# Kernel optimization log

Hardware: AMD Instinct MI355X
Metric: run time of the kernel (lower is better)

Reference implementation:

```python
import jax, jax.numpy as jnp
import numpy as np

RADIUS = 0.5
K = 32
EPS = 1e-5


def ball_query(pc, new_pc, radius, k):
    """pc [B,3,N], new_pc [B,3,S] -> idx [B,S,k] int32, num [B,S] int32.
    First k in-radius points per query; empty slots filled with the first
    found index (standard ball-query semantics of QueryDepthPoint)."""
    d2 = jnp.sum((new_pc[:, :, :, None] - pc[:, :, None, :]) ** 2, axis=1)  # [B,S,N]
    B, S, N = d2.shape
    mask = d2 < radius * radius
    rank = jnp.cumsum(mask.astype(jnp.int32), axis=-1) - 1          # rank among valid
    slot = jnp.where(mask & (rank < k), rank, k)                     # k = dummy slot
    jidx = jnp.broadcast_to(jnp.arange(N, dtype=jnp.int32), (B, S, N))
    bidx = jnp.arange(B)[:, None, None]
    sidx = jnp.arange(S)[None, :, None]
    idx = jnp.zeros((B, S, k + 1), jnp.int32).at[bidx, sidx, slot].set(jidx)
    idx = idx[..., :k]
    num = jnp.sum(mask, axis=-1).astype(jnp.int32)                   # [B,S]
    nvalid = jnp.minimum(num, k)
    idx = jnp.where(jnp.arange(k) < nvalid[..., None], idx, idx[..., :1])
    return idx, num


def conv_bn_relu(x, w, b, g, be):
    """1x1 Conv2d + BatchNorm2d (batch stats, training mode) + ReLU.
    x [B,Cin,S,K], w [Cout,Cin]."""
    y = jnp.einsum('bcsk,oc->bosk', x, w) + b[None, :, None, None]
    mean = jnp.mean(y, axis=(0, 2, 3), keepdims=True)
    var = jnp.var(y, axis=(0, 2, 3), keepdims=True)
    y = (y - mean) * jax.lax.rsqrt(var + EPS) * g[None, :, None, None] + be[None, :, None, None]
    return jax.nn.relu(y)


def setup_inputs() -> dict:
    key = jax.random.key(0)
    ks = jax.random.split(key, 8)
    B, N, S, C = 4, 8192, 2048, 16
    mlp = [32, 32, 64]
    cin = C + 3  # use_xyz concat
    pc = jax.random.normal(ks[0], (B, 3, N), jnp.float32)
    feat = jax.random.normal(ks[1], (B, C, N), jnp.float32)
    new_pc = jax.random.normal(ks[2], (B, 3, S), jnp.float32)
    def kaiming(k, co, ci):
        return jax.random.normal(k, (co, ci), jnp.float32) * np.sqrt(2.0 / ci)
    w1 = kaiming(ks[3], mlp[0], cin)
    w2 = kaiming(ks[4], mlp[1], mlp[0])
    w3 = kaiming(ks[5], mlp[2], mlp[1])
    return {
        'pc': pc, 'feat': feat, 'new_pc': new_pc,
        'w1': w1, 'b1': jnp.zeros((mlp[0],)), 'g1': jnp.ones((mlp[0],)), 'be1': jnp.zeros((mlp[0],)),
        'w2': w2, 'b2': jnp.zeros((mlp[1],)), 'g2': jnp.ones((mlp[1],)), 'be2': jnp.zeros((mlp[1],)),
        'w3': w3, 'b3': jnp.zeros((mlp[2],)), 'g3': jnp.ones((mlp[2],)), 'be3': jnp.zeros((mlp[2],)),
    }


def reference(pc, feat, new_pc, w1, b1, g1, be1, w2, b2, g2, be2, w3, b3, g3, be3):
    B = pc.shape[0]
    S = new_pc.shape[2]
    idx, num = ball_query(pc, new_pc, RADIUS, K)          # [B,S,K], [B,S]
    bidx = jnp.arange(B)[:, None, None]
    # gather neighbors: fancy index -> [B,S,K,3] / [B,S,K,Cf], then to channel-first
    grouped_pc = pc[bidx, :, idx].transpose(0, 3, 1, 2)   # [B,3,S,K]
    grouped_pc = grouped_pc - new_pc[:, :, :, None]       # center on query
    grouped_feat = feat[bidx, :, idx].transpose(0, 3, 1, 2)  # [B,Cf,S,K]
    x = jnp.concatenate([grouped_pc, grouped_feat], axis=1)  # [B,Cf+3,S,K]
    x = conv_bn_relu(x, w1, b1, g1, be1)
    x = conv_bn_relu(x, w2, b2, g2, be2)
    x = conv_bn_relu(x, w3, b3, g3, be3)
    valid = (num > 0).astype(x.dtype)[:, None, :, None]   # [B,1,S,1]
    return x * valid
```

## Files before the change

### kernel.cpp

```cpp
#include <hip/hip_runtime.h>

#define BQ_RADIUS2 0.25f
#define KK 32
#define NB 4
#define NP 8192
#define NS 2048
#define C1 32
#define C2 32
#define C3 64
#define EPSBN 1e-5f
#define RTOT 65536
#define MTOT (NB*NS*KK)
#define NSLOT 32

#define OFF_G     0
#define OFF_IDX   655360
#define OFF_VALID 917504
#define OFF_P1    925696
#define OFF_P2    927744
#define OFF_P3    929792
#define OFF_PAR1  933888
#define OFF_PAR2  933952
#define OFF_PAR3  934016

__global__ __launch_bounds__(256) void k_pack(const float* __restrict__ pc,
                                              const float* __restrict__ feat,
                                              float* __restrict__ g,
                                              float* __restrict__ partials) {
  const int t = blockIdx.x * 256 + threadIdx.x;
  if (t < 8192) partials[t] = 0.f;
  const int b = t >> 13;
  const int j = t & (NP - 1);
  const float* pcb = pc + b * 3 * NP;
  float* gp = g + (size_t)t * 20;
  gp[0] = pcb[j];
  gp[1] = pcb[NP + j];
  gp[2] = pcb[2 * NP + j];
  const float* fb = feat + b * 16 * NP;
#pragma unroll
  for (int c = 0; c < 16; c++) gp[3 + c] = fb[c * NP + j];
  gp[19] = 0.f;
}

__global__ __launch_bounds__(256) void k_ballquery(const float* __restrict__ pc,
                                                   const float* __restrict__ newpc,
                                                   int* __restrict__ idx,
                                                   int* __restrict__ valid) {
  __shared__ int buf[4][KK];
  const int tid = threadIdx.x;
  const int w = tid >> 6, lane = tid & 63;
  const int gq = blockIdx.x * 4 + w;
  const int b = gq >> 11, s = gq & (NS - 1);
  const float* np0 = newpc + b * 3 * NS;
  const float qx = np0[s], qy = np0[NS + s], qz = np0[2 * NS + s];
  const float* px = pc + b * 3 * NP;
  const float* py = px + NP;
  const float* pz = px + 2 * NP;
  if (lane == 0) buf[w][0] = 0;
  int cnt = 0;
  for (int j0 = 0; j0 < NP; j0 += 256) {
    const int jb = j0 + lane * 4;
    const float4 vx = *(const float4*)(px + jb);
    const float4 vy = *(const float4*)(py + jb);
    const float4 vz = *(const float4*)(pz + jb);
    int mm = 0;
    {
      float dx = __fsub_rn(qx, vx.x), dy = __fsub_rn(qy, vy.x), dz = __fsub_rn(qz, vz.x);
      if (__fadd_rn(__fadd_rn(__fmul_rn(dx, dx), __fmul_rn(dy, dy)), __fmul_rn(dz, dz)) < BQ_RADIUS2) mm |= 1;
    }
    {
      float dx = __fsub_rn(qx, vx.y), dy = __fsub_rn(qy, vy.y), dz = __fsub_rn(qz, vz.y);
      if (__fadd_rn(__fadd_rn(__fmul_rn(dx, dx), __fmul_rn(dy, dy)), __fmul_rn(dz, dz)) < BQ_RADIUS2) mm |= 2;
    }
    {
      float dx = __fsub_rn(qx, vx.z), dy = __fsub_rn(qy, vy.z), dz = __fsub_rn(qz, vz.z);
      if (__fadd_rn(__fadd_rn(__fmul_rn(dx, dx), __fmul_rn(dy, dy)), __fmul_rn(dz, dz)) < BQ_RADIUS2) mm |= 4;
    }
    {
      float dx = __fsub_rn(qx, vx.w), dy = __fsub_rn(qy, vy.w), dz = __fsub_rn(qz, vz.w);
      if (__fadd_rn(__fadd_rn(__fmul_rn(dx, dx), __fmul_rn(dy, dy)), __fmul_rn(dz, dz)) < BQ_RADIUS2) mm |= 8;
    }
    const int c4 = __popc(mm);
    int pre = c4;
#pragma unroll
    for (int off = 1; off < 64; off <<= 1) {
      int v = __shfl_up(pre, off);
      if (lane >= off) pre += v;
    }
    const int total = __shfl(pre, 63);
    if (mm) {
      int base = cnt + pre - c4;
#pragma unroll
      for (int i = 0; i < 4; i++) {
        if ((mm >> i) & 1) {
          if (base < KK) buf[w][base] = jb + i;
          base++;
        }
      }
    }
    cnt += total;
    if (cnt >= KK) break;
  }
  __syncthreads();
  if (lane < KK) {
    const int f = cnt < KK ? cnt : KK;
    const int i0 = buf[w][0];
    idx[gq * KK + lane] = (lane < f) ? buf[w][lane] : i0;
  }
  if (lane == 0) valid[gq] = (cnt > 0);
}

__global__ __launch_bounds__(256, 1) void k_conv1(const float* __restrict__ g,
                                                  const int* __restrict__ idx,
                                                  const float* __restrict__ newpc,
                                                  const float* __restrict__ w1,
                                                  const float* __restrict__ b1,
                                                  float* __restrict__ y,
                                                  float* __restrict__ partial) {
  __shared__ float wl[C1 * 20];
  __shared__ float bl[C1];
  __shared__ float red[16][2 * C1 + 1];
  const int tid = threadIdx.x;
  for (int i = tid; i < C1 * 20; i += 256) {
    const int o = i / 20, c = i - o * 20;
    wl[i] = (c < 19) ? w1[o * 19 + c] : 0.f;
  }
  if (tid < C1) bl[tid] = b1[tid];
  __syncthreads();
  const int pos = blockIdx.x * 256 + tid;
  const int p4 = pos << 2;
  const int b = p4 >> 16;
  const int r = p4 & (RTOT - 1);
  const int s = r >> 5;
  const int4 jj = *(const int4*)(idx + p4);
  const float* np0 = newpc + b * 3 * NS;
  const float nx = np0[s], ny = np0[NS + s], nz = np0[2 * NS + s];
  float4 xr[20];
#define LOADPT(COMP, J) { \
    const float4* gp = (const float4*)(g + (size_t)(b * NP + (J)) * 20); \
    const float4 a0 = gp[0], a1 = gp[1], a2 = gp[2], a3 = gp[3], a4 = gp[4]; \
    xr[0].COMP = a0.x - nx; xr[1].COMP = a0.y - ny; xr[2].COMP = a0.z - nz; xr[3].COMP = a0.w; \
    xr[4].COMP = a1.x; xr[5].COMP = a1.y; xr[6].COMP = a1.z; xr[7].COMP = a1.w; \
    xr[8].COMP = a2.x; xr[9].COMP = a2.y; xr[10].COMP = a2.z; xr[11].COMP = a2.w; \
    xr[12].COMP = a3.x; xr[13].COMP = a3.y; xr[14].COMP = a3.z; xr[15].COMP = a3.w; \
    xr[16].COMP = a4.x; xr[17].COMP = a4.y; xr[18].COMP = a4.z; xr[19].COMP = a4.w; }
  LOADPT(x, jj.x) LOADPT(y, jj.y) LOADPT(z, jj.z) LOADPT(w, jj.w)
#undef LOADPT
  float* yb = y + ((size_t)b * C3) * RTOT + r;
  const int grp = tid >> 4;
  const bool lead = (tid & 15) == 0;
#pragma unroll 4
  for (int o = 0; o < C1; o++) {
    const float bo = bl[o];
    float4 acc = make_float4(bo, bo, bo, bo);
    const float4* wr = (const float4*)&wl[o * 20];
#pragma unroll
    for (int ct = 0; ct < 5; ct++) {
      const float4 wv = wr[ct];
      const float4 x0 = xr[4 * ct + 0], x1 = xr[4 * ct + 1], x2 = xr[4 * ct + 2], x3 = xr[4 * ct + 3];
      acc.x = fmaf(wv.x, x0.x, acc.x); acc.y = fmaf(wv.x, x0.y, acc.y);
      acc.z = fmaf(wv.x, x0.z, acc.z); acc.w = fmaf(wv.x, x0.w, acc.w);
      acc.x = fmaf(wv.y, x1.x, acc.x); acc.y = fmaf(wv.y, x1.y, acc.y);
      acc.z = fmaf(wv.y, x1.z, acc.z); acc.w = fmaf(wv.y, x1.w, acc.w);
      acc.x = fmaf(wv.z, x2.x, acc.x); acc.y = fmaf(wv.z, x2.y, acc.y);
      acc.z = fmaf(wv.z, x2.z, acc.z); acc.w = fmaf(wv.z, x2.w, acc.w);
      acc.x = fmaf(wv.w, x3.x, acc.x); acc.y = fmaf(wv.w, x3.y, acc.y);
      acc.z = fmaf(wv.w, x3.z, acc.z); acc.w = fmaf(wv.w, x3.w, acc.w);
    }
    *(float4*)(yb + (size_t)o * RTOT) = acc;
    float a = (acc.x + acc.y) + (acc.z + acc.w);
    float q = (acc.x * acc.x + acc.y * acc.y) + (acc.z * acc.z + acc.w * acc.w);
    a += __shfl_xor(a, 1); q += __shfl_xor(q, 1);
    a += __shfl_xor(a, 2); q += __shfl_xor(q, 2);
    a += __shfl_xor(a, 4); q += __shfl_xor(q, 4);
    a += __shfl_xor(a, 8); q += __shfl_xor(q, 8);
    if (lead) { red[grp][o] = a; red[grp][C1 + o] = q; }
  }
  __syncthreads();
  if (tid < 2 * C1) {
    float v = 0.f;
#pragma unroll
    for (int gq = 0; gq < 16; gq++) v += red[gq][tid];
    atomicAdd(&partial[(blockIdx.x & (NSLOT - 1)) * 2 * C1 + tid], v);
  }
}

__global__ __launch_bounds__(256, 1) void k_conv2(const float* __restrict__ w2,
                                                  const float* __restrict__ b2,
                                                  const float* __restrict__ par,
                                                  float* y,
                                                  float* __restrict__ partial) {
  __shared__ float wl[C2 * C1];
  __shared__ float bl[C2];
  __shared__ float pl[2 * C1];
  __shared__ float red[16][2 * C2 + 1];
  const int tid = threadIdx.x;
  for (int i = tid; i < C2 * C1; i += 256) wl[i] = w2[i];
  if (tid < C2) bl[tid] = b2[tid];
  if (tid < 2 * C1) pl[tid] = par[tid];
  __syncthreads();
  const int pos = blockIdx.x * 256 + tid;
  const int p4 = pos << 2;
  const int b = p4 >> 16;
  const int r = p4 & (RTOT - 1);
  float* yb = y + ((size_t)b * C3) * RTOT + r;
  float4 xr[C1];
#pragma unroll
  for (int c = 0; c < C1; c++) {
    float4 v = *(const float4*)(yb + (size_t)c * RTOT);
    const float sc = pl[c], sh = pl[C1 + c];
    v.x = fmaxf(fmaf(v.x, sc, sh), 0.f);
    v.y = fmaxf(fmaf(v.y, sc, sh), 0.f);
    v.z = fmaxf(fmaf(v.z, sc, sh), 0.f);
    v.w = fmaxf(fmaf(v.w, sc, sh), 0.f);
    xr[c] = v;
  }
  const int grp = tid >> 4;
  const bool lead = (tid & 15) == 0;
#pragma unroll 4
  for (int o = 0; o < C2; o++) {
    const float bo = bl[o];
    float4 acc = make_float4(bo, bo, bo, bo);
    const float4* wr = (const float4*)&wl[o * C1];
#pragma unroll
    for (int ct = 0; ct < C1 / 4; ct++) {
      const float4 wv = wr[ct];
      const float4 x0 = xr[4 * ct + 0], x1 = xr[4 * ct + 1], x2 = xr[4 * ct + 2], x3 = xr[4 * ct + 3];
      acc.x = fmaf(wv.x, x0.x, acc.x); acc.y = fmaf(wv.x, x0.y, acc.y);
      acc.z = fmaf(wv.x, x0.z, acc.z); acc.w = fmaf(wv.x, x0.w, acc.w);
      acc.x = fmaf(wv.y, x1.x, acc.x); acc.y = fmaf(wv.y, x1.y, acc.y);
      acc.z = fmaf(wv.y, x1.z, acc.z); acc.w = fmaf(wv.y, x1.w, acc.w);
      acc.x = fmaf(wv.z, x2.x, acc.x); acc.y = fmaf(wv.z, x2.y, acc.y);
      acc.z = fmaf(wv.z, x2.z, acc.z); acc.w = fmaf(wv.z, x2.w, acc.w);
      acc.x = fmaf(wv.w, x3.x, acc.x); acc.y = fmaf(wv.w, x3.y, acc.y);
      acc.z = fmaf(wv.w, x3.z, acc.z); acc.w = fmaf(wv.w, x3.w, acc.w);
    }
    *(float4*)(yb + (size_t)o * RTOT) = acc;
    float a = (acc.x + acc.y) + (acc.z + acc.w);
    float q = (acc.x * acc.x + acc.y * acc.y) + (acc.z * acc.z + acc.w * acc.w);
    a += __shfl_xor(a, 1); q += __shfl_xor(q, 1);
    a += __shfl_xor(a, 2); q += __shfl_xor(q, 2);
    a += __shfl_xor(a, 4); q += __shfl_xor(q, 4);
    a += __shfl_xor(a, 8); q += __shfl_xor(q, 8);
    if (lead) { red[grp][o] = a; red[grp][C2 + o] = q; }
  }
  __syncthreads();
  if (tid < 2 * C2) {
    float v = 0.f;
#pragma unroll
    for (int gq = 0; gq < 16; gq++) v += red[gq][tid];
    atomicAdd(&partial[(blockIdx.x & (NSLOT - 1)) * 2 * C2 + tid], v);
  }
}

__global__ __launch_bounds__(256, 1) void k_conv3(const float* __restrict__ w3,
                                                  const float* __restrict__ b3,
                                                  const float* __restrict__ par,
                                                  float* y,
                                                  float* __restrict__ partial) {
  __shared__ float wl[C3 * C2];
  __shared__ float bl[C3];
  __shared__ float pl[2 * C2];
  __shared__ float red[16][2 * C3 + 1];
  const int tid = threadIdx.x;
  for (int i = tid; i < C3 * C2; i += 256) wl[i] = w3[i];
  if (tid < C3) bl[tid] = b3[tid];
  if (tid < 2 * C2) pl[tid] = par[tid];
  __syncthreads();
  const int pos = blockIdx.x * 256 + tid;
  const int p4 = pos << 2;
  const int b = p4 >> 16;
  const int r = p4 & (RTOT - 1);
  float* yb = y + ((size_t)b * C3) * RTOT + r;
  float4 xr[C2];
#pragma unroll
  for (int c = 0; c < C2; c++) {
    float4 v = *(const float4*)(yb + (size_t)c * RTOT);
    const float sc = pl[c], sh = pl[C2 + c];
    v.x = fmaxf(fmaf(v.x, sc, sh), 0.f);
    v.y = fmaxf(fmaf(v.y, sc, sh), 0.f);
    v.z = fmaxf(fmaf(v.z, sc, sh), 0.f);
    v.w = fmaxf(fmaf(v.w, sc, sh), 0.f);
    xr[c] = v;
  }
  const int grp = tid >> 4;
  const bool lead = (tid & 15) == 0;
#pragma unroll 4
  for (int o = 0; o < C3; o++) {
    const float bo = bl[o];
    float4 acc = make_float4(bo, bo, bo, bo);
    const float4* wr = (const float4*)&wl[o * C2];
#pragma unroll
    for (int ct = 0; ct < C2 / 4; ct++) {
      const float4 wv = wr[ct];
      const float4 x0 = xr[4 * ct + 0], x1 = xr[4 * ct + 1], x2 = xr[4 * ct + 2], x3 = xr[4 * ct + 3];
      acc.x = fmaf(wv.x, x0.x, acc.x); acc.y = fmaf(wv.x, x0.y, acc.y);
      acc.z = fmaf(wv.x, x0.z, acc.z); acc.w = fmaf(wv.x, x0.w, acc.w);
      acc.x = fmaf(wv.y, x1.x, acc.x); acc.y = fmaf(wv.y, x1.y, acc.y);
      acc.z = fmaf(wv.y, x1.z, acc.z); acc.w = fmaf(wv.y, x1.w, acc.w);
      acc.x = fmaf(wv.z, x2.x, acc.x); acc.y = fmaf(wv.z, x2.y, acc.y);
      acc.z = fmaf(wv.z, x2.z, acc.z); acc.w = fmaf(wv.z, x2.w, acc.w);
      acc.x = fmaf(wv.w, x3.x, acc.x); acc.y = fmaf(wv.w, x3.y, acc.y);
      acc.z = fmaf(wv.w, x3.z, acc.z); acc.w = fmaf(wv.w, x3.w, acc.w);
    }
    *(float4*)(yb + (size_t)o * RTOT) = acc;
    float a = (acc.x + acc.y) + (acc.z + acc.w);
    float q = (acc.x * acc.x + acc.y * acc.y) + (acc.z * acc.z + acc.w * acc.w);
    a += __shfl_xor(a, 1); q += __shfl_xor(q, 1);
    a += __shfl_xor(a, 2); q += __shfl_xor(q, 2);
    a += __shfl_xor(a, 4); q += __shfl_xor(q, 4);
    a += __shfl_xor(a, 8); q += __shfl_xor(q, 8);
    if (lead) { red[grp][o] = a; red[grp][C3 + o] = q; }
  }
  __syncthreads();
  if (tid < 2 * C3) {
    float v = 0.f;
#pragma unroll
    for (int gq = 0; gq < 16; gq++) v += red[gq][tid];
    atomicAdd(&partial[(blockIdx.x & (NSLOT - 1)) * 2 * C3 + tid], v);
  }
}

__global__ void k_params(const float* __restrict__ partial,
                         const float* __restrict__ gamma,
                         const float* __restrict__ beta,
                         float* __restrict__ params, int C) {
  __shared__ float tot[2 * C3];
  const int t = threadIdx.x;
  float v = 0.f;
#pragma unroll 1
  for (int sl = 0; sl < NSLOT; ++sl) v += partial[sl * 2 * C + t];
  tot[t] = v;
  __syncthreads();
  if (t < C) {
    const float inv = 1.0f / (float)MTOT;
    const float mean = tot[t] * inv;
    const float ex2 = tot[C + t] * inv;
    const float var = ex2 - mean * mean;
    const float sc = gamma[t] * rsqrtf(var + EPSBN);
    params[t] = sc;
    params[C + t] = beta[t] - mean * sc;
  }
}

__global__ __launch_bounds__(256) void k_final(float* __restrict__ out,
                                               const float* __restrict__ par,
                                               const int* __restrict__ valid) {
  const int t = blockIdx.x * 256 + threadIdx.x;
  const size_t e = (size_t)t * 4;
  const int b = t >> 20;
  const int o = (t >> 14) & 63;
  const int s = (t & 16383) >> 3;
  const float sc = par[o], sh = par[C3 + o];
  const float m = valid[(b << 11) + s] ? 1.f : 0.f;
  float4 v = *(float4*)(out + e);
  v.x = fmaxf(fmaf(v.x, sc, sh), 0.f) * m;
  v.y = fmaxf(fmaf(v.y, sc, sh), 0.f) * m;
  v.z = fmaxf(fmaf(v.z, sc, sh), 0.f) * m;
  v.w = fmaxf(fmaf(v.w, sc, sh), 0.f) * m;
  *(float4*)(out + e) = v;
}

extern "C" void kernel_launch(void* const* d_in, const int* in_sizes, int n_in,
                              void* d_out, int out_size, void* d_ws, size_t ws_size,
                              hipStream_t stream) {
  const float* pc    = (const float*)d_in[0];
  const float* feat  = (const float*)d_in[1];
  const float* newpc = (const float*)d_in[2];
  const float* w1 = (const float*)d_in[3];
  const float* b1 = (const float*)d_in[4];
  const float* g1 = (const float*)d_in[5];
  const float* be1 = (const float*)d_in[6];
  const float* w2 = (const float*)d_in[7];
  const float* b2 = (const float*)d_in[8];
  const float* g2 = (const float*)d_in[9];
  const float* be2 = (const float*)d_in[10];
  const float* w3 = (const float*)d_in[11];
  const float* b3 = (const float*)d_in[12];
  const float* g3 = (const float*)d_in[13];
  const float* be3 = (const float*)d_in[14];

  float* ws = (float*)d_ws;
  float* gbuf  = ws + OFF_G;
  int*   idx   = (int*)(ws + OFF_IDX);
  int*   valid = (int*)(ws + OFF_VALID);
  float* p1 = ws + OFF_P1;
  float* p2 = ws + OFF_P2;
  float* p3 = ws + OFF_P3;
  float* par1 = ws + OFF_PAR1;
  float* par2 = ws + OFF_PAR2;
  float* par3 = ws + OFF_PAR3;
  float* out = (float*)d_out;

  k_pack<<<dim3(128), dim3(256), 0, stream>>>(pc, feat, gbuf, p1);
  k_ballquery<<<dim3(2048), dim3(256), 0, stream>>>(pc, newpc, idx, valid);
  k_conv1<<<dim3(256), dim3(256), 0, stream>>>(gbuf, idx, newpc, w1, b1, out, p1);
  k_params<<<dim3(1), dim3(2 * C1), 0, stream>>>(p1, g1, be1, par1, C1);
  k_conv2<<<dim3(256), dim3(256), 0, stream>>>(w2, b2, par1, out, p2);
  k_params<<<dim3(1), dim3(2 * C2), 0, stream>>>(p2, g2, be2, par2, C2);
  k_conv3<<<dim3(256), dim3(256), 0, stream>>>(w3, b3, par2, out, p3);
  k_params<<<dim3(1), dim3(2 * C3), 0, stream>>>(p3, g3, be3, par3, C3);
  k_final<<<dim3(16384), dim3(256), 0, stream>>>(out, par3, valid);
}
```

Before: 247.6 us.

## Split conv output channels across waves and fold BN params into next conv

Each 256-thread block of the three conv kernels now covers 64 position-quads instead of 256. Its four waves each compute a quarter of the output channels for the same positions, which quadruples the grid to 1024 blocks and allows two blocks per CU. The aim is more occupancy and better latency hiding than one block per CU gave. The separate k_params launches after conv1 and conv2 are removed: every block recomputes the BN scale and shift from the partial sums, which saves two tiny serial launches. The cost is redundant gathers and input reads across the four waves, plus an extra barrier before the in-place overwrite of the activations.

```diff
diff --git a/kernel.cpp b/kernel.cpp
--- a/kernel.cpp
+++ b/kernel.cpp
@@ -110,7 +110,7 @@
   if (lane == 0) valid[gq] = (cnt > 0);
 }
 
-__global__ __launch_bounds__(256, 1) void k_conv1(const float* __restrict__ g,
+__global__ __launch_bounds__(256, 2) void k_conv1(const float* __restrict__ g,
                                                   const int* __restrict__ idx,
                                                   const float* __restrict__ newpc,
                                                   const float* __restrict__ w1,
@@ -119,7 +119,7 @@
                                                   float* __restrict__ partial) {
   __shared__ float wl[C1 * 20];
   __shared__ float bl[C1];
-  __shared__ float red[16][2 * C1 + 1];
+  __shared__ float red[2 * C1];
   const int tid = threadIdx.x;
   for (int i = tid; i < C1 * 20; i += 256) {
     const int o = i / 20, c = i - o * 20;
@@ -127,8 +127,9 @@
   }
   if (tid < C1) bl[tid] = b1[tid];
   __syncthreads();
-  const int pos = blockIdx.x * 256 + tid;
-  const int p4 = pos << 2;
+  const int w = tid >> 6, lane = tid & 63;
+  const int cg = blockIdx.x * 64 + lane;
+  const int p4 = cg << 2;
   const int b = p4 >> 16;
   const int r = p4 & (RTOT - 1);
   const int s = r >> 5;
@@ -147,10 +148,10 @@
   LOADPT(x, jj.x) LOADPT(y, jj.y) LOADPT(z, jj.z) LOADPT(w, jj.w)
 #undef LOADPT
   float* yb = y + ((size_t)b * C3) * RTOT + r;
-  const int grp = tid >> 4;
-  const bool lead = (tid & 15) == 0;
+  const int o0 = w * (C1 / 4);
 #pragma unroll 4
-  for (int o = 0; o < C1; o++) {
+  for (int oi = 0; oi < C1 / 4; oi++) {
+    const int o = o0 + oi;
     const float bo = bl[o];
     float4 acc = make_float4(bo, bo, bo, bo);
     const float4* wr = (const float4*)&wl[o * 20];
@@ -170,37 +171,53 @@
     *(float4*)(yb + (size_t)o * RTOT) = acc;
     float a = (acc.x + acc.y) + (acc.z + acc.w);
     float q = (acc.x * acc.x + acc.y * acc.y) + (acc.z * acc.z + acc.w * acc.w);
-    a += __shfl_xor(a, 1); q += __shfl_xor(q, 1);
-    a += __shfl_xor(a, 2); q += __shfl_xor(q, 2);
-    a += __shfl_xor(a, 4); q += __shfl_xor(q, 4);
-    a += __shfl_xor(a, 8); q += __shfl_xor(q, 8);
-    if (lead) { red[grp][o] = a; red[grp][C1 + o] = q; }
-  }
-  __syncthreads();
-  if (tid < 2 * C1) {
-    float v = 0.f;
-#pragma unroll
-    for (int gq = 0; gq < 16; gq++) v += red[gq][tid];
-    atomicAdd(&partial[(blockIdx.x & (NSLOT - 1)) * 2 * C1 + tid], v);
-  }
-}
-
-__global__ __launch_bounds__(256, 1) void k_conv2(const float* __restrict__ w2,
+    a += __shfl_xor(a, 1);  q += __shfl_xor(q, 1);
+    a += __shfl_xor(a, 2);  q += __shfl_xor(q, 2);
+    a += __shfl_xor(a, 4);  q += __shfl_xor(q, 4);
+    a += __shfl_xor(a, 8);  q += __shfl_xor(q, 8);
+    a += __shfl_xor(a, 16); q += __shfl_xor(q, 16);
+    a += __shfl_xor(a, 32); q += __shfl_xor(q, 32);
+    if (lane == 0) { red[o] = a; red[C1 + o] = q; }
+  }
+  __syncthreads();
+  if (tid < 2 * C1)
+    atomicAdd(&partial[(blockIdx.x & (NSLOT - 1)) * 2 * C1 + tid], red[tid]);
+}
+
+__global__ __launch_bounds__(256, 2) void k_conv2(const float* __restrict__ w2,
                                                   const float* __restrict__ b2,
-                                                  const float* __restrict__ par,
+                                                  const float* __restrict__ p1,
+                                                  const float* __restrict__ g1,
+                                                  const float* __restrict__ be1,
                                                   float* y,
                                                   float* __restrict__ partial) {
   __shared__ float wl[C2 * C1];
   __shared__ float bl[C2];
   __shared__ float pl[2 * C1];
-  __shared__ float red[16][2 * C2 + 1];
+  __shared__ float tot[2 * C1];
+  __shared__ float red[2 * C2];
   const int tid = threadIdx.x;
   for (int i = tid; i < C2 * C1; i += 256) wl[i] = w2[i];
   if (tid < C2) bl[tid] = b2[tid];
-  if (tid < 2 * C1) pl[tid] = par[tid];
-  __syncthreads();
-  const int pos = blockIdx.x * 256 + tid;
-  const int p4 = pos << 2;
+  if (tid < 2 * C1) {
+    float v = 0.f;
+#pragma unroll 1
+    for (int sl = 0; sl < NSLOT; ++sl) v += p1[sl * 2 * C1 + tid];
+    tot[tid] = v;
+  }
+  __syncthreads();
+  if (tid < C1) {
+    const float inv = 1.0f / (float)MTOT;
+    const float mean = tot[tid] * inv;
+    const float var = tot[C1 + tid] * inv - mean * mean;
+    const float sc = g1[tid] * rsqrtf(var + EPSBN);
+    pl[tid] = sc;
+    pl[C1 + tid] = be1[tid] - mean * sc;
+  }
+  __syncthreads();
+  const int w = tid >> 6, lane = tid & 63;
+  const int cg = blockIdx.x * 64 + lane;
+  const int p4 = cg << 2;
   const int b = p4 >> 16;
   const int r = p4 & (RTOT - 1);
   float* yb = y + ((size_t)b * C3) * RTOT + r;
@@ -215,10 +232,11 @@
     v.w = fmaxf(fmaf(v.w, sc, sh), 0.f);
     xr[c] = v;
   }
-  const int grp = tid >> 4;
-  const bool lead = (tid & 15) == 0;
+  __syncthreads();
+  const int o0 = w * (C2 / 4);
 #pragma unroll 4
-  for (int o = 0; o < C2; o++) {
+  for (int oi = 0; oi < C2 / 4; oi++) {
+    const int o = o0 + oi;
     const float bo = bl[o];
     float4 acc = make_float4(bo, bo, bo, bo);
     const float4* wr = (const float4*)&wl[o * C1];
@@ -238,37 +256,53 @@
     *(float4*)(yb + (size_t)o * RTOT) = acc;
     float a = (acc.x + acc.y) + (acc.z + acc.w);
     float q = (acc.x * acc.x + acc.y * acc.y) + (acc.z * acc.z + acc.w * acc.w);
-    a += __shfl_xor(a, 1); q += __shfl_xor(q, 1);
-    a += __shfl_xor(a, 2); q += __shfl_xor(q, 2);
-    a += __shfl_xor(a, 4); q += __shfl_xor(q, 4);
-    a += __shfl_xor(a, 8); q += __shfl_xor(q, 8);
-    if (lead) { red[grp][o] = a; red[grp][C2 + o] = q; }
-  }
-  __syncthreads();
-  if (tid < 2 * C2) {
-    float v = 0.f;
-#pragma unroll
-    for (int gq = 0; gq < 16; gq++) v += red[gq][tid];
-    atomicAdd(&partial[(blockIdx.x & (NSLOT - 1)) * 2 * C2 + tid], v);
-  }
-}
-
-__global__ __launch_bounds__(256, 1) void k_conv3(const float* __restrict__ w3,
+    a += __shfl_xor(a, 1);  q += __shfl_xor(q, 1);
+    a += __shfl_xor(a, 2);  q += __shfl_xor(q, 2);
+    a += __shfl_xor(a, 4);  q += __shfl_xor(q, 4);
+    a += __shfl_xor(a, 8);  q += __shfl_xor(q, 8);
+    a += __shfl_xor(a, 16); q += __shfl_xor(q, 16);
+    a += __shfl_xor(a, 32); q += __shfl_xor(q, 32);
+    if (lane == 0) { red[o] = a; red[C2 + o] = q; }
+  }
+  __syncthreads();
+  if (tid < 2 * C2)
+    atomicAdd(&partial[(blockIdx.x & (NSLOT - 1)) * 2 * C2 + tid], red[tid]);
+}
+
+__global__ __launch_bounds__(256, 2) void k_conv3(const float* __restrict__ w3,
                                                   const float* __restrict__ b3,
-                                                  const float* __restrict__ par,
+                                                  const float* __restrict__ p2,
+                                                  const float* __restrict__ g2,
+                                                  const float* __restrict__ be2,
                                                   float* y,
                                                   float* __restrict__ partial) {
   __shared__ float wl[C3 * C2];
   __shared__ float bl[C3];
   __shared__ float pl[2 * C2];
-  __shared__ float red[16][2 * C3 + 1];
+  __shared__ float tot[2 * C2];
+  __shared__ float red[2 * C3];
   const int tid = threadIdx.x;
   for (int i = tid; i < C3 * C2; i += 256) wl[i] = w3[i];
   if (tid < C3) bl[tid] = b3[tid];
-  if (tid < 2 * C2) pl[tid] = par[tid];
-  __syncthreads();
-  const int pos = blockIdx.x * 256 + tid;
-  const int p4 = pos << 2;
+  if (tid < 2 * C2) {
+    float v = 0.f;
+#pragma unroll 1
+    for (int sl = 0; sl < NSLOT; ++sl) v += p2[sl * 2 * C2 + tid];
+    tot[tid] = v;
+  }
+  __syncthreads();
+  if (tid < C2) {
+    const float inv = 1.0f / (float)MTOT;
+    const float mean = tot[tid] * inv;
+    const float var = tot[C2 + tid] * inv - mean * mean;
+    const float sc = g2[tid] * rsqrtf(var + EPSBN);
+    pl[tid] = sc;
+    pl[C2 + tid] = be2[tid] - mean * sc;
+  }
+  __syncthreads();
+  const int w = tid >> 6, lane = tid & 63;
+  const int cg = blockIdx.x * 64 + lane;
+  const int p4 = cg << 2;
   const int b = p4 >> 16;
   const int r = p4 & (RTOT - 1);
   float* yb = y + ((size_t)b * C3) * RTOT + r;
@@ -283,10 +317,11 @@
     v.w = fmaxf(fmaf(v.w, sc, sh), 0.f);
     xr[c] = v;
   }
-  const int grp = tid >> 4;
-  const bool lead = (tid & 15) == 0;
+  __syncthreads();
+  const int o0 = w * (C3 / 4);
 #pragma unroll 4
-  for (int o = 0; o < C3; o++) {
+  for (int oi = 0; oi < C3 / 4; oi++) {
+    const int o = o0 + oi;
     const float bo = bl[o];
     float4 acc = make_float4(bo, bo, bo, bo);
     const float4* wr = (const float4*)&wl[o * C2];
@@ -306,19 +341,17 @@
     *(float4*)(yb + (size_t)o * RTOT) = acc;
     float a = (acc.x + acc.y) + (acc.z + acc.w);
     float q = (acc.x * acc.x + acc.y * acc.y) + (acc.z * acc.z + acc.w * acc.w);
-    a += __shfl_xor(a, 1); q += __shfl_xor(q, 1);
-    a += __shfl_xor(a, 2); q += __shfl_xor(q, 2);
-    a += __shfl_xor(a, 4); q += __shfl_xor(q, 4);
-    a += __shfl_xor(a, 8); q += __shfl_xor(q, 8);
-    if (lead) { red[grp][o] = a; red[grp][C3 + o] = q; }
-  }
-  __syncthreads();
-  if (tid < 2 * C3) {
-    float v = 0.f;
-#pragma unroll
-    for (int gq = 0; gq < 16; gq++) v += red[gq][tid];
-    atomicAdd(&partial[(blockIdx.x & (NSLOT - 1)) * 2 * C3 + tid], v);
-  }
+    a += __shfl_xor(a, 1);  q += __shfl_xor(q, 1);
+    a += __shfl_xor(a, 2);  q += __shfl_xor(q, 2);
+    a += __shfl_xor(a, 4);  q += __shfl_xor(q, 4);
+    a += __shfl_xor(a, 8);  q += __shfl_xor(q, 8);
+    a += __shfl_xor(a, 16); q += __shfl_xor(q, 16);
+    a += __shfl_xor(a, 32); q += __shfl_xor(q, 32);
+    if (lane == 0) { red[o] = a; red[C3 + o] = q; }
+  }
+  __syncthreads();
+  if (tid < 2 * C3)
+    atomicAdd(&partial[(blockIdx.x & (NSLOT - 1)) * 2 * C3 + tid], red[tid]);
 }
 
 __global__ void k_params(const float* __restrict__ partial,
@@ -387,18 +420,14 @@
   float* p1 = ws + OFF_P1;
   float* p2 = ws + OFF_P2;
   float* p3 = ws + OFF_P3;
-  float* par1 = ws + OFF_PAR1;
-  float* par2 = ws + OFF_PAR2;
   float* par3 = ws + OFF_PAR3;
   float* out = (float*)d_out;
 
   k_pack<<<dim3(128), dim3(256), 0, stream>>>(pc, feat, gbuf, p1);
   k_ballquery<<<dim3(2048), dim3(256), 0, stream>>>(pc, newpc, idx, valid);
-  k_conv1<<<dim3(256), dim3(256), 0, stream>>>(gbuf, idx, newpc, w1, b1, out, p1);
-  k_params<<<dim3(1), dim3(2 * C1), 0, stream>>>(p1, g1, be1, par1, C1);
-  k_conv2<<<dim3(256), dim3(256), 0, stream>>>(w2, b2, par1, out, p2);
-  k_params<<<dim3(1), dim3(2 * C2), 0, stream>>>(p2, g2, be2, par2, C2);
-  k_conv3<<<dim3(256), dim3(256), 0, stream>>>(w3, b3, par2, out, p3);
+  k_conv1<<<dim3(1024), dim3(256), 0, stream>>>(gbuf, idx, newpc, w1, b1, out, p1);
+  k_conv2<<<dim3(1024), dim3(256), 0, stream>>>(w2, b2, p1, g1, be1, out, p2);
+  k_conv3<<<dim3(1024), dim3(256), 0, stream>>>(w3, b3, p2, g2, be2, out, p3);
   k_params<<<dim3(1), dim3(2 * C3), 0, stream>>>(p3, g3, be3, par3, C3);
   k_final<<<dim3(16384), dim3(256), 0, stream>>>(out, par3, valid);
 }
```

Result: slower. 258.5 us (+4.4%).

## Fuse conv/BN stages into one persistent kernel with grid-wide barriers

Applied to the files above, without the earlier changes.

Replaces the three conv kernels, three BN-param kernels and the final activation kernel with a single persistent kernel of 256 blocks × 1024 threads. Each thread keeps one point's activations in registers across all three layers, and a software grid barrier on an atomic counter separates the batch-statistics reductions. This removes the intermediate global writes and reads of y and the extra launches. In exchange it relies on all 256 blocks being co-resident, carries about 128 live floats per thread, reads weights from global instead of shared memory, and writes output with one scalar store per element.

```diff
diff --git a/kernel.cpp b/kernel.cpp
--- a/kernel.cpp
+++ b/kernel.cpp
@@ -12,6 +12,7 @@
 #define RTOT 65536
 #define MTOT (NB*NS*KK)
 #define NSLOT 32
+#define NBLK 256
 
 #define OFF_G     0
 #define OFF_IDX   655360
@@ -19,16 +20,14 @@
 #define OFF_P1    925696
 #define OFF_P2    927744
 #define OFF_P3    929792
-#define OFF_PAR1  933888
-#define OFF_PAR2  933952
-#define OFF_PAR3  934016
+#define OFF_BAR   933888
 
 __global__ __launch_bounds__(256) void k_pack(const float* __restrict__ pc,
                                               const float* __restrict__ feat,
                                               float* __restrict__ g,
                                               float* __restrict__ partials) {
   const int t = blockIdx.x * 256 + threadIdx.x;
-  if (t < 8192) partials[t] = 0.f;
+  if (t < 8194) partials[t] = 0.f;
   const int b = t >> 13;
   const int j = t & (NP - 1);
   const float* pcb = pc + b * 3 * NP;
@@ -110,255 +109,158 @@
   if (lane == 0) valid[gq] = (cnt > 0);
 }
 
-__global__ __launch_bounds__(256, 1) void k_conv1(const float* __restrict__ g,
-                                                  const int* __restrict__ idx,
-                                                  const float* __restrict__ newpc,
-                                                  const float* __restrict__ w1,
-                                                  const float* __restrict__ b1,
-                                                  float* __restrict__ y,
-                                                  float* __restrict__ partial) {
-  __shared__ float wl[C1 * 20];
-  __shared__ float bl[C1];
-  __shared__ float red[16][2 * C1 + 1];
+__device__ __forceinline__ void gbar(int* bar, int tid) {
+  __syncthreads();
+  if (tid == 0) {
+    __threadfence();
+    int* gen = bar + 1;
+    const int g = __hip_atomic_load(gen, __ATOMIC_ACQUIRE, __HIP_MEMORY_SCOPE_AGENT);
+    const int a = __hip_atomic_fetch_add(bar, 1, __ATOMIC_ACQ_REL, __HIP_MEMORY_SCOPE_AGENT);
+    if (a == NBLK - 1) {
+      __hip_atomic_store(bar, 0, __ATOMIC_RELAXED, __HIP_MEMORY_SCOPE_AGENT);
+      __hip_atomic_fetch_add(gen, 1, __ATOMIC_RELEASE, __HIP_MEMORY_SCOPE_AGENT);
+    } else {
+      while (__hip_atomic_load(gen, __ATOMIC_ACQUIRE, __HIP_MEMORY_SCOPE_AGENT) == g)
+        __builtin_amdgcn_s_sleep(8);
+    }
+  }
+  __syncthreads();
+}
+
+template <int C>
+__device__ __forceinline__ void block_stats(const float* y, float (*red)[16],
+                                            float* __restrict__ partial,
+                                            int tid, int bid) {
+  const int w = tid >> 6, lane = tid & 63;
+#pragma unroll
+  for (int c = 0; c < C; c++) {
+    float a = y[c];
+    float q = a * a;
+    a += __shfl_xor(a, 1);  q += __shfl_xor(q, 1);
+    a += __shfl_xor(a, 2);  q += __shfl_xor(q, 2);
+    a += __shfl_xor(a, 4);  q += __shfl_xor(q, 4);
+    a += __shfl_xor(a, 8);  q += __shfl_xor(q, 8);
+    a += __shfl_xor(a, 16); q += __shfl_xor(q, 16);
+    a += __shfl_xor(a, 32); q += __shfl_xor(q, 32);
+    if (lane == 0) { red[c][w] = a; red[C + c][w] = q; }
+  }
+  __syncthreads();
+  if (tid < 2 * C) {
+    float v = 0.f;
+#pragma unroll
+    for (int ww = 0; ww < 16; ww++) v += red[tid][ww];
+    atomicAdd(&partial[(bid & (NSLOT - 1)) * 2 * C + tid], v);
+  }
+}
+
+template <int C>
+__device__ __forceinline__ void bn_params(const float* __restrict__ partial,
+                                          const float* __restrict__ gam,
+                                          const float* __restrict__ bet,
+                                          float* pl, float* tot, int tid) {
+  if (tid < 2 * C) {
+    float v = 0.f;
+#pragma unroll 1
+    for (int sl = 0; sl < NSLOT; ++sl) v += partial[sl * 2 * C + tid];
+    tot[tid] = v;
+  }
+  __syncthreads();
+  if (tid < C) {
+    const float inv = 1.0f / (float)MTOT;
+    const float mean = tot[tid] * inv;
+    const float var = tot[C + tid] * inv - mean * mean;
+    const float sc = gam[tid] * rsqrtf(var + EPSBN);
+    pl[tid] = sc;
+    pl[C + tid] = bet[tid] - mean * sc;
+  }
+  __syncthreads();
+}
+
+__global__ __launch_bounds__(1024, 4) void k_mega(
+    const float* __restrict__ g, const int* __restrict__ idx,
+    const float* __restrict__ newpc,
+    const float* __restrict__ w1, const float* __restrict__ b1,
+    const float* __restrict__ g1, const float* __restrict__ be1,
+    const float* __restrict__ w2, const float* __restrict__ b2,
+    const float* __restrict__ g2, const float* __restrict__ be2,
+    const float* __restrict__ w3, const float* __restrict__ b3,
+    const float* __restrict__ g3, const float* __restrict__ be3,
+    const int* __restrict__ valid,
+    float* __restrict__ p1, float* __restrict__ p2, float* __restrict__ p3,
+    float* __restrict__ out, int* bar) {
+  __shared__ float red[2 * C3][16];
+  __shared__ float tot[2 * C3];
+  __shared__ float pl[2 * C3];
   const int tid = threadIdx.x;
-  for (int i = tid; i < C1 * 20; i += 256) {
-    const int o = i / 20, c = i - o * 20;
-    wl[i] = (c < 19) ? w1[o * 19 + c] : 0.f;
-  }
-  if (tid < C1) bl[tid] = b1[tid];
-  __syncthreads();
-  const int pos = blockIdx.x * 256 + tid;
-  const int p4 = pos << 2;
-  const int b = p4 >> 16;
-  const int r = p4 & (RTOT - 1);
+  const int bid = blockIdx.x;
+
+  const int m = bid * 1024 + tid;
+  const int b = m >> 16;
+  const int r = m & (RTOT - 1);
   const int s = r >> 5;
-  const int4 jj = *(const int4*)(idx + p4);
+  const int j = idx[m];
   const float* np0 = newpc + b * 3 * NS;
-  const float nx = np0[s], ny = np0[NS + s], nz = np0[2 * NS + s];
-  float4 xr[20];
-#define LOADPT(COMP, J) { \
-    const float4* gp = (const float4*)(g + (size_t)(b * NP + (J)) * 20); \
-    const float4 a0 = gp[0], a1 = gp[1], a2 = gp[2], a3 = gp[3], a4 = gp[4]; \
-    xr[0].COMP = a0.x - nx; xr[1].COMP = a0.y - ny; xr[2].COMP = a0.z - nz; xr[3].COMP = a0.w; \
-    xr[4].COMP = a1.x; xr[5].COMP = a1.y; xr[6].COMP = a1.z; xr[7].COMP = a1.w; \
-    xr[8].COMP = a2.x; xr[9].COMP = a2.y; xr[10].COMP = a2.z; xr[11].COMP = a2.w; \
-    xr[12].COMP = a3.x; xr[13].COMP = a3.y; xr[14].COMP = a3.z; xr[15].COMP = a3.w; \
-    xr[16].COMP = a4.x; xr[17].COMP = a4.y; xr[18].COMP = a4.z; xr[19].COMP = a4.w; }
-  LOADPT(x, jj.x) LOADPT(y, jj.y) LOADPT(z, jj.z) LOADPT(w, jj.w)
-#undef LOADPT
-  float* yb = y + ((size_t)b * C3) * RTOT + r;
-  const int grp = tid >> 4;
-  const bool lead = (tid & 15) == 0;
-#pragma unroll 4
+
+  float x[19];
+  {
+    const float4* gp = (const float4*)(g + (size_t)(b * NP + j) * 20);
+    const float4 a0 = gp[0], a1 = gp[1], a2 = gp[2], a3 = gp[3], a4 = gp[4];
+    x[0] = a0.x - np0[s]; x[1] = a0.y - np0[NS + s]; x[2] = a0.z - np0[2 * NS + s];
+    x[3] = a0.w;
+    x[4] = a1.x; x[5] = a1.y; x[6] = a1.z; x[7] = a1.w;
+    x[8] = a2.x; x[9] = a2.y; x[10] = a2.z; x[11] = a2.w;
+    x[12] = a3.x; x[13] = a3.y; x[14] = a3.z; x[15] = a3.w;
+    x[16] = a4.x; x[17] = a4.y; x[18] = a4.z;
+  }
+
+  float y1[C1];
+#pragma unroll
   for (int o = 0; o < C1; o++) {
-    const float bo = bl[o];
-    float4 acc = make_float4(bo, bo, bo, bo);
-    const float4* wr = (const float4*)&wl[o * 20];
-#pragma unroll
-    for (int ct = 0; ct < 5; ct++) {
-      const float4 wv = wr[ct];
-      const float4 x0 = xr[4 * ct + 0], x1 = xr[4 * ct + 1], x2 = xr[4 * ct + 2], x3 = xr[4 * ct + 3];
-      acc.x = fmaf(wv.x, x0.x, acc.x); acc.y = fmaf(wv.x, x0.y, acc.y);
-      acc.z = fmaf(wv.x, x0.z, acc.z); acc.w = fmaf(wv.x, x0.w, acc.w);
-      acc.x = fmaf(wv.y, x1.x, acc.x); acc.y = fmaf(wv.y, x1.y, acc.y);
-      acc.z = fmaf(wv.y, x1.z, acc.z); acc.w = fmaf(wv.y, x1.w, acc.w);
-      acc.x = fmaf(wv.z, x2.x, acc.x); acc.y = fmaf(wv.z, x2.y, acc.y);
-      acc.z = fmaf(wv.z, x2.z, acc.z); acc.w = fmaf(wv.z, x2.w, acc.w);
-      acc.x = fmaf(wv.w, x3.x, acc.x); acc.y = fmaf(wv.w, x3.y, acc.y);
-      acc.z = fmaf(wv.w, x3.z, acc.z); acc.w = fmaf(wv.w, x3.w, acc.w);
-    }
-    *(float4*)(yb + (size_t)o * RTOT) = acc;
-    float a = (acc.x + acc.y) + (acc.z + acc.w);
-    float q = (acc.x * acc.x + acc.y * acc.y) + (acc.z * acc.z + acc.w * acc.w);
-    a += __shfl_xor(a, 1); q += __shfl_xor(q, 1);
-    a += __shfl_xor(a, 2); q += __shfl_xor(q, 2);
-    a += __shfl_xor(a, 4); q += __shfl_xor(q, 4);
-    a += __shfl_xor(a, 8); q += __shfl_xor(q, 8);
-    if (lead) { red[grp][o] = a; red[grp][C1 + o] = q; }
-  }
-  __syncthreads();
-  if (tid < 2 * C1) {
-    float v = 0.f;
-#pragma unroll
-    for (int gq = 0; gq < 16; gq++) v += red[gq][tid];
-    atomicAdd(&partial[(blockIdx.x & (NSLOT - 1)) * 2 * C1 + tid], v);
-  }
-}
-
-__global__ __launch_bounds__(256, 1) void k_conv2(const float* __restrict__ w2,
-                                                  const float* __restrict__ b2,
-                                                  const float* __restrict__ par,
-                                                  float* y,
-                                                  float* __restrict__ partial) {
-  __shared__ float wl[C2 * C1];
-  __shared__ float bl[C2];
-  __shared__ float pl[2 * C1];
-  __shared__ float red[16][2 * C2 + 1];
-  const int tid = threadIdx.x;
-  for (int i = tid; i < C2 * C1; i += 256) wl[i] = w2[i];
-  if (tid < C2) bl[tid] = b2[tid];
-  if (tid < 2 * C1) pl[tid] = par[tid];
-  __syncthreads();
-  const int pos = blockIdx.x * 256 + tid;
-  const int p4 = pos << 2;
-  const int b = p4 >> 16;
-  const int r = p4 & (RTOT - 1);
-  float* yb = y + ((size_t)b * C3) * RTOT + r;
-  float4 xr[C1];
-#pragma unroll
-  for (int c = 0; c < C1; c++) {
-    float4 v = *(const float4*)(yb + (size_t)c * RTOT);
-    const float sc = pl[c], sh = pl[C1 + c];
-    v.x = fmaxf(fmaf(v.x, sc, sh), 0.f);
-    v.y = fmaxf(fmaf(v.y, sc, sh), 0.f);
-    v.z = fmaxf(fmaf(v.z, sc, sh), 0.f);
-    v.w = fmaxf(fmaf(v.w, sc, sh), 0.f);
-    xr[c] = v;
-  }
-  const int grp = tid >> 4;
-  const bool lead = (tid & 15) == 0;
-#pragma unroll 4
+    float acc = b1[o];
+    const float* wr = w1 + o * 19;
+#pragma unroll
+    for (int c = 0; c < 19; c++) acc = fmaf(wr[c], x[c], acc);
+    y1[o] = acc;
+  }
+  block_stats<C1>(y1, red, p1, tid, bid);
+  gbar(bar, tid);
+
+  bn_params<C1>(p1, g1, be1, pl, tot, tid);
+#pragma unroll
+  for (int c = 0; c < C1; c++) y1[c] = fmaxf(fmaf(y1[c], pl[c], pl[C1 + c]), 0.f);
+  float y2[C2];
+#pragma unroll
   for (int o = 0; o < C2; o++) {
-    const float bo = bl[o];
-    float4 acc = make_float4(bo, bo, bo, bo);
-    const float4* wr = (const float4*)&wl[o * C1];
-#pragma unroll
-    for (int ct = 0; ct < C1 / 4; ct++) {
-      const float4 wv = wr[ct];
-      const float4 x0 = xr[4 * ct + 0], x1 = xr[4 * ct + 1], x2 = xr[4 * ct + 2], x3 = xr[4 * ct + 3];
-      acc.x = fmaf(wv.x, x0.x, acc.x); acc.y = fmaf(wv.x, x0.y, acc.y);
-      acc.z = fmaf(wv.x, x0.z, acc.z); acc.w = fmaf(wv.x, x0.w, acc.w);
-      acc.x = fmaf(wv.y, x1.x, acc.x); acc.y = fmaf(wv.y, x1.y, acc.y);
-      acc.z = fmaf(wv.y, x1.z, acc.z); acc.w = fmaf(wv.y, x1.w, acc.w);
-      acc.x = fmaf(wv.z, x2.x, acc.x); acc.y = fmaf(wv.z, x2.y, acc.y);
-      acc.z = fmaf(wv.z, x2.z, acc.z); acc.w = fmaf(wv.z, x2.w, acc.w);
-      acc.x = fmaf(wv.w, x3.x, acc.x); acc.y = fmaf(wv.w, x3.y, acc.y);
-      acc.z = fmaf(wv.w, x3.z, acc.z); acc.w = fmaf(wv.w, x3.w, acc.w);
-    }
-    *(float4*)(yb + (size_t)o * RTOT) = acc;
-    float a = (acc.x + acc.y) + (acc.z + acc.w);
-    float q = (acc.x * acc.x + acc.y * acc.y) + (acc.z * acc.z + acc.w * acc.w);
-    a += __shfl_xor(a, 1); q += __shfl_xor(q, 1);
-    a += __shfl_xor(a, 2); q += __shfl_xor(q, 2);
-    a += __shfl_xor(a, 4); q += __shfl_xor(q, 4);
-    a += __shfl_xor(a, 8); q += __shfl_xor(q, 8);
-    if (lead) { red[grp][o] = a; red[grp][C2 + o] = q; }
-  }
-  __syncthreads();
-  if (tid < 2 * C2) {
-    float v = 0.f;
-#pragma unroll
-    for (int gq = 0; gq < 16; gq++) v += red[gq][tid];
-    atomicAdd(&partial[(blockIdx.x & (NSLOT - 1)) * 2 * C2 + tid], v);
-  }
-}
-
-__global__ __launch_bounds__(256, 1) void k_conv3(const float* __restrict__ w3,
-                                                  const float* __restrict__ b3,
-                                                  const float* __restrict__ par,
-                                                  float* y,
-                                                  float* __restrict__ partial) {
-  __shared__ float wl[C3 * C2];
-  __shared__ float bl[C3];
-  __shared__ float pl[2 * C2];
-  __shared__ float red[16][2 * C3 + 1];
-  const int tid = threadIdx.x;
-  for (int i = tid; i < C3 * C2; i += 256) wl[i] = w3[i];
-  if (tid < C3) bl[tid] = b3[tid];
-  if (tid < 2 * C2) pl[tid] = par[tid];
-  __syncthreads();
-  const int pos = blockIdx.x * 256 + tid;
-  const int p4 = pos << 2;
-  const int b = p4 >> 16;
-  const int r = p4 & (RTOT - 1);
-  float* yb = y + ((size_t)b * C3) * RTOT + r;
-  float4 xr[C2];
-#pragma unroll
-  for (int c = 0; c < C2; c++) {
-    float4 v = *(const float4*)(yb + (size_t)c * RTOT);
-    const float sc = pl[c], sh = pl[C2 + c];
-    v.x = fmaxf(fmaf(v.x, sc, sh), 0.f);
-    v.y = fmaxf(fmaf(v.y, sc, sh), 0.f);
-    v.z = fmaxf(fmaf(v.z, sc, sh), 0.f);
-    v.w = fmaxf(fmaf(v.w, sc, sh), 0.f);
-    xr[c] = v;
-  }
-  const int grp = tid >> 4;
-  const bool lead = (tid & 15) == 0;
-#pragma unroll 4
+    float acc = b2[o];
+    const float* wr = w2 + o * C1;
+#pragma unroll
+    for (int c = 0; c < C1; c++) acc = fmaf(wr[c], y1[c], acc);
+    y2[o] = acc;
+  }
+  block_stats<C2>(y2, red, p2, tid, bid);
+  gbar(bar, tid);
+
+  bn_params<C2>(p2, g2, be2, pl, tot, tid);
+#pragma unroll
+  for (int c = 0; c < C2; c++) y2[c] = fmaxf(fmaf(y2[c], pl[c], pl[C2 + c]), 0.f);
+  float y3[C3];
+#pragma unroll
   for (int o = 0; o < C3; o++) {
-    const float bo = bl[o];
-    float4 acc = make_float4(bo, bo, bo, bo);
-    const float4* wr = (const float4*)&wl[o * C2];
-#pragma unroll
-    for (int ct = 0; ct < C2 / 4; ct++) {
-      const float4 wv = wr[ct];
-      const float4 x0 = xr[4 * ct + 0], x1 = xr[4 * ct + 1], x2 = xr[4 * ct + 2], x3 = xr[4 * ct + 3];
-      acc.x = fmaf(wv.x, x0.x, acc.x); acc.y = fmaf(wv.x, x0.y, acc.y);
-      acc.z = fmaf(wv.x, x0.z, acc.z); acc.w = fmaf(wv.x, x0.w, acc.w);
-      acc.x = fmaf(wv.y, x1.x, acc.x); acc.y = fmaf(wv.y, x1.y, acc.y);
-      acc.z = fmaf(wv.y, x1.z, acc.z); acc.w = fmaf(wv.y, x1.w, acc.w);
-      acc.x = fmaf(wv.z, x2.x, acc.x); acc.y = fmaf(wv.z, x2.y, acc.y);
-      acc.z = fmaf(wv.z, x2.z, acc.z); acc.w = fmaf(wv.z, x2.w, acc.w);
-      acc.x = fmaf(wv.w, x3.x, acc.x); acc.y = fmaf(wv.w, x3.y, acc.y);
-      acc.z = fmaf(wv.w, x3.z, acc.z); acc.w = fmaf(wv.w, x3.w, acc.w);
-    }
-    *(float4*)(yb + (size_t)o * RTOT) = acc;
-    float a = (acc.x + acc.y) + (acc.z + acc.w);
-    float q = (acc.x * acc.x + acc.y * acc.y) + (acc.z * acc.z + acc.w * acc.w);
-    a += __shfl_xor(a, 1); q += __shfl_xor(q, 1);
-    a += __shfl_xor(a, 2); q += __shfl_xor(q, 2);
-    a += __shfl_xor(a, 4); q += __shfl_xor(q, 4);
-    a += __shfl_xor(a, 8); q += __shfl_xor(q, 8);
-    if (lead) { red[grp][o] = a; red[grp][C3 + o] = q; }
-  }
-  __syncthreads();
-  if (tid < 2 * C3) {
-    float v = 0.f;
-#pragma unroll
-    for (int gq = 0; gq < 16; gq++) v += red[gq][tid];
-    atomicAdd(&partial[(blockIdx.x & (NSLOT - 1)) * 2 * C3 + tid], v);
-  }
-}
-
-__global__ void k_params(const float* __restrict__ partial,
-                         const float* __restrict__ gamma,
-                         const float* __restrict__ beta,
-                         float* __restrict__ params, int C) {
-  __shared__ float tot[2 * C3];
-  const int t = threadIdx.x;
-  float v = 0.f;
-#pragma unroll 1
-  for (int sl = 0; sl < NSLOT; ++sl) v += partial[sl * 2 * C + t];
-  tot[t] = v;
-  __syncthreads();
-  if (t < C) {
-    const float inv = 1.0f / (float)MTOT;
-    const float mean = tot[t] * inv;
-    const float ex2 = tot[C + t] * inv;
-    const float var = ex2 - mean * mean;
-    const float sc = gamma[t] * rsqrtf(var + EPSBN);
-    params[t] = sc;
-    params[C + t] = beta[t] - mean * sc;
-  }
-}
-
-__global__ __launch_bounds__(256) void k_final(float* __restrict__ out,
-                                               const float* __restrict__ par,
-                                               const int* __restrict__ valid) {
-  const int t = blockIdx.x * 256 + threadIdx.x;
-  const size_t e = (size_t)t * 4;
-  const int b = t >> 20;
-  const int o = (t >> 14) & 63;
-  const int s = (t & 16383) >> 3;
-  const float sc = par[o], sh = par[C3 + o];
-  const float m = valid[(b << 11) + s] ? 1.f : 0.f;
-  float4 v = *(float4*)(out + e);
-  v.x = fmaxf(fmaf(v.x, sc, sh), 0.f) * m;
-  v.y = fmaxf(fmaf(v.y, sc, sh), 0.f) * m;
-  v.z = fmaxf(fmaf(v.z, sc, sh), 0.f) * m;
-  v.w = fmaxf(fmaf(v.w, sc, sh), 0.f) * m;
-  *(float4*)(out + e) = v;
+    float acc = b3[o];
+    const float* wr = w3 + o * C2;
+#pragma unroll
+    for (int c = 0; c < C2; c++) acc = fmaf(wr[c], y2[c], acc);
+    y3[o] = acc;
+  }
+  block_stats<C3>(y3, red, p3, tid, bid);
+  gbar(bar, tid);
+
+  bn_params<C3>(p3, g3, be3, pl, tot, tid);
+  const float mval = valid[(b << 11) + s] ? 1.f : 0.f;
+  float* ob = out + ((size_t)b * C3) * RTOT + r;
+#pragma unroll
+  for (int o = 0; o < C3; o++)
+    ob[(size_t)o * RTOT] = fmaxf(fmaf(y3[o], pl[o], pl[C3 + o]), 0.f) * mval;
 }
 
 extern "C" void kernel_launch(void* const* d_in, const int* in_sizes, int n_in,
@@ -387,18 +289,12 @@
   float* p1 = ws + OFF_P1;
   float* p2 = ws + OFF_P2;
   float* p3 = ws + OFF_P3;
-  float* par1 = ws + OFF_PAR1;
-  float* par2 = ws + OFF_PAR2;
-  float* par3 = ws + OFF_PAR3;
+  int*   bar = (int*)(ws + OFF_BAR);
   float* out = (float*)d_out;
 
   k_pack<<<dim3(128), dim3(256), 0, stream>>>(pc, feat, gbuf, p1);
   k_ballquery<<<dim3(2048), dim3(256), 0, stream>>>(pc, newpc, idx, valid);
-  k_conv1<<<dim3(256), dim3(256), 0, stream>>>(gbuf, idx, newpc, w1, b1, out, p1);
-  k_params<<<dim3(1), dim3(2 * C1), 0, stream>>>(p1, g1, be1, par1, C1);
-  k_conv2<<<dim3(256), dim3(256), 0, stream>>>(w2, b2, par1, out, p2);
-  k_params<<<dim3(1), dim3(2 * C2), 0, stream>>>(p2, g2, be2, par2, C2);
-  k_conv3<<<dim3(256), dim3(256), 0, stream>>>(w3, b3, par2, out, p3);
-  k_params<<<dim3(1), dim3(2 * C3), 0, stream>>>(p3, g3, be3, par3, C3);
-  k_final<<<dim3(16384), dim3(256), 0, stream>>>(out, par3, valid);
-}
+  k_mega<<<dim3(NBLK), dim3(1024), 0, stream>>>(
+      gbuf, idx, newpc, w1, b1, g1, be1, w2, b2, g2, be2, w3, b3, g3, be3,
+      valid, p1, p2, p3, out, bar);
+}
```

Result: slower. 322.5 us (+30.2%).
